# Optimization experiments

Hardware: AMD Instinct MI355X
Metric: run time of the kernel (lower is better)

The kernel has to match this reference:

```python
import jax, jax.numpy as jnp
import numpy as np

N = 50000
NEG_SLOPE = 0.2


def gat_conv(x, src, dst, W, a_src, a_dst, b):
    # PyG GATConv, heads=1: h = xW; e_ij = LeakyReLU(a_src.h_j + a_dst.h_i);
    # softmax over edges sharing destination i; out_i = sum_j alpha_ij h_j + b.
    h = x @ W                                   # [N, F]
    as_ = h @ a_src                             # [N]
    ad_ = h @ a_dst                             # [N]
    e = jax.nn.leaky_relu(as_[src] + ad_[dst], NEG_SLOPE)  # [E]
    m = jax.ops.segment_max(e, dst, num_segments=N)        # per-dst max
    m = jnp.where(jnp.isfinite(m), m, 0.0)
    p = jnp.exp(e - m[dst])
    denom = jax.ops.segment_sum(p, dst, num_segments=N)
    alpha = p / jnp.maximum(denom[dst], 1e-16)             # [E]
    out = jax.ops.segment_sum(alpha[:, None] * h[src], dst, num_segments=N)
    return out + b


def setup_inputs() -> dict:
    key = jax.random.key(0)
    ks = jax.random.split(key, 12)
    E, L = 800000, 262144
    F_in, F_mid, F_out = 128, 64, 32
    x = jax.random.normal(ks[0], (N, F_in), dtype=jnp.float32)
    edge_index = jax.random.randint(ks[1], (2, E), 0, N, dtype=jnp.int32)
    edge_label_index = jax.random.randint(ks[2], (2, L), 0, N, dtype=jnp.int32)
    s1 = 1.0 / np.sqrt(F_in)
    s2 = 1.0 / np.sqrt(F_mid)
    return {
        "x": x,
        "edge_index": edge_index,
        "edge_label_index": edge_label_index,
        "W1": jax.random.normal(ks[3], (F_in, F_mid), jnp.float32) * s1,
        "a_src1": jax.random.normal(ks[4], (F_mid,), jnp.float32) * s2,
        "a_dst1": jax.random.normal(ks[5], (F_mid,), jnp.float32) * s2,
        "b1": jnp.zeros((F_mid,), jnp.float32),
        "W2": jax.random.normal(ks[6], (F_mid, F_out), jnp.float32) * s2,
        "a_src2": jax.random.normal(ks[7], (F_out,), jnp.float32) * (1.0 / np.sqrt(F_out)),
        "a_dst2": jax.random.normal(ks[8], (F_out,), jnp.float32) * (1.0 / np.sqrt(F_out)),
        "b2": jnp.zeros((F_out,), jnp.float32),
    }


def reference(x, edge_index, edge_label_index, W1, a_src1, a_dst1, b1, W2, a_src2, a_dst2, b2):
    # add self-loops (PyG GATConv default add_self_loops=True)
    loops = jnp.arange(N, dtype=edge_index.dtype)
    src = jnp.concatenate([edge_index[0], loops])
    dst = jnp.concatenate([edge_index[1], loops])
    z = jax.nn.relu(gat_conv(x, src, dst, W1, a_src1, a_dst1, b1))
    z = gat_conv(z, src, dst, W2, a_src2, a_dst2, b2)
    # dot-product decode over candidate edges
    return jnp.sum(z[edge_label_index[0]] * z[edge_label_index[1]], axis=-1)
```

## Files before the change

### kernel.cpp

```cpp
#include <hip/hip_runtime.h>

#define NN 50000
#define NEG 0.2f
#define NBUCK 196
#define NBLK 208
#define SLOT 64

__device__ __forceinline__ float leaky(float v) { return v > 0.0f ? v : NEG * v; }

__device__ __forceinline__ unsigned f2bf(float x) {
    unsigned u = __float_as_uint(x);
    return (u + 0x7FFFu + ((u >> 16) & 1u)) >> 16;
}
__device__ __forceinline__ float bflo(unsigned g) { return __uint_as_float(g << 16); }
__device__ __forceinline__ float bfhi(unsigned g) { return __uint_as_float(g & 0xFFFF0000u); }

__global__ __launch_bounds__(256) void k_part_gemm1(
        const int* __restrict__ ei, int E, int CHUNK,
        int* __restrict__ bh, unsigned int* __restrict__ part,
        const float* __restrict__ x, const float* __restrict__ W,
        const float* __restrict__ a_src, const float* __restrict__ a_dst,
        unsigned int* __restrict__ hu, float* __restrict__ as_, float* __restrict__ ad_) {
    __shared__ float xs[4][8][128];
    __shared__ int hist[NBUCK];
    int tid = threadIdx.x;
    if (blockIdx.x < NBLK) {
        int b = blockIdx.x;
        if (tid < NBUCK) hist[tid] = 0;
        __syncthreads();
        int beg = b * CHUNK;
        int end = min(beg + CHUNK, E);
        for (int i = beg + tid; i < end; i += 256) {
            int sv = ei[i], dv = ei[E + i];
            int k = dv >> 8;
            int slot = atomicAdd(&hist[k], 1);
            if (slot < SLOT)
                part[(k * NBLK + b) * SLOT + slot] =
                    (unsigned)sv | ((unsigned)(dv & 255) << 16);
        }
        __syncthreads();
        if (tid < NBUCK) bh[b * NBUCK + tid] = min(hist[tid], SLOT);
        return;
    }
    int gblock = blockIdx.x - NBLK;
    int wl = tid >> 6;
    int lane = tid & 63;
    int base = (gblock * 4 + wl) * 8;
    if (base >= NN) return;
#pragma unroll
    for (int n = 0; n < 8; ++n) {
        int node = base + n;
        xs[wl][n][lane]      = x[node * 128 + lane];
        xs[wl][n][lane + 64] = x[node * 128 + 64 + lane];
    }
    float acc[8] = {0, 0, 0, 0, 0, 0, 0, 0};
#pragma unroll 8
    for (int kg = 0; kg < 32; ++kg) {
        float w0 = W[(4 * kg + 0) * 64 + lane];
        float w1 = W[(4 * kg + 1) * 64 + lane];
        float w2 = W[(4 * kg + 2) * 64 + lane];
        float w3 = W[(4 * kg + 3) * 64 + lane];
#pragma unroll
        for (int n = 0; n < 8; ++n) {
            float4 xv = *(const float4*)&xs[wl][n][kg * 4];
            acc[n] = fmaf(xv.x, w0, fmaf(xv.y, w1, fmaf(xv.z, w2, fmaf(xv.w, w3, acc[n]))));
        }
    }
    float pa = a_src[lane], pd = a_dst[lane];
#pragma unroll
    for (int n = 0; n < 8; ++n) {
        int node = base + n;
        unsigned my = f2bf(acc[n]);
        unsigned nb = __shfl_down(my, 1, 64);
        if ((lane & 1) == 0) hu[node * 32 + (lane >> 1)] = my | (nb << 16);
        float s = acc[n] * pa;
        float d = acc[n] * pd;
#pragma unroll
        for (int off = 32; off > 0; off >>= 1) {
            s += __shfl_xor(s, off, 64);
            d += __shfl_xor(d, off, 64);
        }
        if (lane == 0) { as_[node] = s; ad_[node] = d; }
    }
}

__global__ __launch_bounds__(256) void k_csr(
        const unsigned int* __restrict__ part, const int* __restrict__ bh,
        int2* __restrict__ rc, unsigned short* __restrict__ csr_src) {
    int k = blockIdx.x;
    int tid = threadIdx.x;
    int dst = (k << 8) + tid;
    __shared__ int lhist[256], roff[256], wsum[4];
    lhist[tid] = (dst < NN) ? 1 : 0;
    __syncthreads();
    int rl = 0;
    const unsigned int* myslot = part;
    if (tid < NBLK) {
        rl = bh[tid * NBUCK + k];
        myslot = part + (k * NBLK + tid) * SLOT;
        for (int i = 0; i < rl; ++i) atomicAdd(&lhist[myslot[i] >> 16], 1);
    }
    __syncthreads();
    int lane = tid & 63, w = tid >> 6;
    int v = lhist[tid];
    int inc = v;
#pragma unroll
    for (int off = 1; off < 64; off <<= 1) {
        int t = __shfl_up(inc, off, 64);
        if (lane >= off) inc += t;
    }
    if (lane == 63) wsum[w] = inc;
    __syncthreads();
    int wpre = 0;
    for (int q = 0; q < w; ++q) wpre += wsum[q];
    int excl = wpre + inc - v;
    int cbase = k * NBLK * SLOT;
    roff[tid] = cbase + excl;
    if (dst < NN) rc[dst] = make_int2(cbase + excl, v);
    __syncthreads();
    if (dst < NN) {
        int pos = atomicAdd(&roff[tid], 1);
        csr_src[pos] = (unsigned short)dst;
    }
    if (tid < NBLK) {
        for (int i = 0; i < rl; ++i) {
            unsigned e = myslot[i];
            int pos = atomicAdd(&roff[e >> 16], 1);
            csr_src[pos] = (unsigned short)(e & 0xFFFFu);
        }
    }
}

__global__ __launch_bounds__(256) void k_aggr1g2(
        const int2* __restrict__ rc, const unsigned short* __restrict__ csr_src,
        const float* __restrict__ as_, const float* __restrict__ ad_,
        const unsigned int* __restrict__ hu, const float* __restrict__ b1,
        const float* __restrict__ W2, const float* __restrict__ a2s,
        const float* __restrict__ a2d,
        unsigned int* __restrict__ hu2, float* __restrict__ as2,
        float* __restrict__ ad2) {
    __shared__ float w2s[64 * 32];
    int tid = threadIdx.x;
#pragma unroll
    for (int i = 0; i < 8; ++i) w2s[tid + 256 * i] = W2[tid + 256 * i];
    __syncthreads();
    int f = tid & 15;
    int dst = blockIdx.x * 16 + (tid >> 4);
    int2 rcv = rc[dst];
    int start = rcv.x, deg = rcv.y;
    float ad = ad_[dst];
    float a0 = 0, a1 = 0, a2 = 0, a3 = 0, ssum;

    if (deg <= 32) {
        int nA = min(deg, 16);
        int sA = 0, sB = 0;
        float eA = -1e30f, eB = -1e30f;
        if (f < nA) { sA = csr_src[start + f]; eA = leaky(as_[sA] + ad); }
        if (16 + f < deg) { sB = csr_src[start + 16 + f]; eB = leaky(as_[sB] + ad); }
        float m = fmaxf(eA, eB);
#pragma unroll
        for (int off = 8; off > 0; off >>= 1) m = fmaxf(m, __shfl_xor(m, off, 16));
        float pA = (f < nA) ? __expf(eA - m) : 0.0f;
        float pB = (16 + f < deg) ? __expf(eB - m) : 0.0f;
        ssum = pA + pB;
#pragma unroll
        for (int off = 8; off > 0; off >>= 1) ssum += __shfl_xor(ssum, off, 16);
        int t = 0;
        for (; t + 4 <= nA; t += 4) {
            int s0 = __shfl(sA, t, 16), s1 = __shfl(sA, t + 1, 16);
            int s2 = __shfl(sA, t + 2, 16), s3 = __shfl(sA, t + 3, 16);
            float p0 = __shfl(pA, t, 16), p1 = __shfl(pA, t + 1, 16);
            float p2 = __shfl(pA, t + 2, 16), p3 = __shfl(pA, t + 3, 16);
            uint2 g0 = *(const uint2*)&hu[s0 * 32 + 2 * f];
            uint2 g1 = *(const uint2*)&hu[s1 * 32 + 2 * f];
            uint2 g2 = *(const uint2*)&hu[s2 * 32 + 2 * f];
            uint2 g3 = *(const uint2*)&hu[s3 * 32 + 2 * f];
            a0 = fmaf(p0, bflo(g0.x), a0); a1 = fmaf(p0, bfhi(g0.x), a1);
            a2 = fmaf(p0, bflo(g0.y), a2); a3 = fmaf(p0, bfhi(g0.y), a3);
            a0 = fmaf(p1, bflo(g1.x), a0); a1 = fmaf(p1, bfhi(g1.x), a1);
            a2 = fmaf(p1, bflo(g1.y), a2); a3 = fmaf(p1, bfhi(g1.y), a3);
            a0 = fmaf(p2, bflo(g2.x), a0); a1 = fmaf(p2, bfhi(g2.x), a1);
            a2 = fmaf(p2, bflo(g2.y), a2); a3 = fmaf(p2, bfhi(g2.y), a3);
            a0 = fmaf(p3, bflo(g3.x), a0); a1 = fmaf(p3, bfhi(g3.x), a1);
            a2 = fmaf(p3, bflo(g3.y), a2); a3 = fmaf(p3, bfhi(g3.y), a3);
        }
        for (; t < nA; ++t) {
            int sv = __shfl(sA, t, 16);
            float pv = __shfl(pA, t, 16);
            uint2 g = *(const uint2*)&hu[sv * 32 + 2 * f];
            a0 = fmaf(pv, bflo(g.x), a0); a1 = fmaf(pv, bfhi(g.x), a1);
            a2 = fmaf(pv, bflo(g.y), a2); a3 = fmaf(pv, bfhi(g.y), a3);
        }
        for (t = 16; t < deg; ++t) {
            int sv = __shfl(sB, t - 16, 16);
            float pv = __shfl(pB, t - 16, 16);
            uint2 g = *(const uint2*)&hu[sv * 32 + 2 * f];
            a0 = fmaf(pv, bflo(g.x), a0); a1 = fmaf(pv, bfhi(g.x), a1);
            a2 = fmaf(pv, bflo(g.y), a2); a3 = fmaf(pv, bfhi(g.y), a3);
        }
    } else {
        float m = -1e30f;
        for (int base = 0; base < deg; base += 16) {
            int j = base + f;
            if (j < deg) m = fmaxf(m, leaky(as_[csr_src[start + j]] + ad));
        }
#pragma unroll
        for (int off = 8; off > 0; off >>= 1) m = fmaxf(m, __shfl_xor(m, off, 16));
        ssum = 0.0f;
        for (int base = 0; base < deg; base += 16) {
            int j = base + f;
            int sj = 0;
            float pj = 0.0f;
            if (j < deg) {
                sj = csr_src[start + j];
                pj = __expf(leaky(as_[sj] + ad) - m);
            }
            ssum += pj;
            int lim = min(16, deg - base);
            for (int t = 0; t < lim; ++t) {
                int sv = __shfl(sj, t, 16);
                float pv = __shfl(pj, t, 16);
                uint2 g = *(const uint2*)&hu[sv * 32 + 2 * f];
                a0 = fmaf(pv, bflo(g.x), a0); a1 = fmaf(pv, bfhi(g.x), a1);
                a2 = fmaf(pv, bflo(g.y), a2); a3 = fmaf(pv, bfhi(g.y), a3);
            }
        }
#pragma unroll
        for (int off = 8; off > 0; off >>= 1) ssum += __shfl_xor(ssum, off, 16);
    }

    float inv = 1.0f / ssum;
    float4 bb = *(const float4*)&b1[4 * f];
    float z0 = fmaxf(fmaf(a0, inv, bb.x), 0.0f);
    float z1 = fmaxf(fmaf(a1, inv, bb.y), 0.0f);
    float z2 = fmaxf(fmaf(a2, inv, bb.z), 0.0f);
    float z3 = fmaxf(fmaf(a3, inv, bb.w), 0.0f);

    float h0 = 0.0f, h1 = 0.0f;
#pragma unroll 4
    for (int t = 0; t < 16; ++t) {
        float y0 = __shfl(z0, t, 16);
        float y1 = __shfl(z1, t, 16);
        float y2 = __shfl(z2, t, 16);
        float y3 = __shfl(z3, t, 16);
        const float2* wp = (const float2*)&w2s[(4 * t) * 32 + 2 * f];
        float2 w0v = wp[0];
        float2 w1v = wp[16];
        float2 w2v = wp[32];
        float2 w3v = wp[48];
        h0 = fmaf(y0, w0v.x, fmaf(y1, w1v.x, fmaf(y2, w2v.x, fmaf(y3, w3v.x, h0))));
        h1 = fmaf(y0, w0v.y, fmaf(y1, w1v.y, fmaf(y2, w2v.y, fmaf(y3, w3v.y, h1))));
    }
    float2 av = *(const float2*)&a2s[2 * f];
    float2 dv = *(const float2*)&a2d[2 * f];
    float sa = fmaf(h0, av.x, h1 * av.y);
    float sd = fmaf(h0, dv.x, h1 * dv.y);
#pragma unroll
    for (int off = 8; off > 0; off >>= 1) {
        sa += __shfl_xor(sa, off, 16);
        sd += __shfl_xor(sd, off, 16);
    }
    if (f == 0) { as2[dst] = sa; ad2[dst] = sd; }
    hu2[dst * 16 + f] = f2bf(h0) | (f2bf(h1) << 16);
}

__global__ void k_aggr2(const int2* __restrict__ rc,
                        const unsigned short* __restrict__ csr_src,
                        const float* __restrict__ as_, const float* __restrict__ ad_,
                        const unsigned int* __restrict__ hu2, const float* __restrict__ b,
                        float* __restrict__ out) {
    int gid = blockIdx.x * blockDim.x + threadIdx.x;
    int dst = gid >> 4;
    int f = gid & 15;
    if (dst >= NN) return;
    int2 rcv = rc[dst];
    int start = rcv.x, deg = rcv.y;
    float ad = ad_[dst];
    float a0 = 0, a1 = 0, ssum;

    if (deg <= 32) {
        int nA = min(deg, 16);
        int sA = 0, sB = 0;
        float eA = -1e30f, eB = -1e30f;
        if (f < nA) { sA = csr_src[start + f]; eA = leaky(as_[sA] + ad); }
        if (16 + f < deg) { sB = csr_src[start + 16 + f]; eB = leaky(as_[sB] + ad); }
        float m = fmaxf(eA, eB);
#pragma unroll
        for (int off = 8; off > 0; off >>= 1) m = fmaxf(m, __shfl_xor(m, off, 16));
        float pA = (f < nA) ? __expf(eA - m) : 0.0f;
        float pB = (16 + f < deg) ? __expf(eB - m) : 0.0f;
        ssum = pA + pB;
#pragma unroll
        for (int off = 8; off > 0; off >>= 1) ssum += __shfl_xor(ssum, off, 16);
        int t = 0;
        for (; t + 4 <= nA; t += 4) {
            int s0 = __shfl(sA, t, 16), s1 = __shfl(sA, t + 1, 16);
            int s2 = __shfl(sA, t + 2, 16), s3 = __shfl(sA, t + 3, 16);
            float p0 = __shfl(pA, t, 16), p1 = __shfl(pA, t + 1, 16);
            float p2 = __shfl(pA, t + 2, 16), p3 = __shfl(pA, t + 3, 16);
            unsigned g0 = hu2[s0 * 16 + f];
            unsigned g1 = hu2[s1 * 16 + f];
            unsigned g2 = hu2[s2 * 16 + f];
            unsigned g3 = hu2[s3 * 16 + f];
            a0 = fmaf(p0, bflo(g0), a0); a1 = fmaf(p0, bfhi(g0), a1);
            a0 = fmaf(p1, bflo(g1), a0); a1 = fmaf(p1, bfhi(g1), a1);
            a0 = fmaf(p2, bflo(g2), a0); a1 = fmaf(p2, bfhi(g2), a1);
            a0 = fmaf(p3, bflo(g3), a0); a1 = fmaf(p3, bfhi(g3), a1);
        }
        for (; t < nA; ++t) {
            int sv = __shfl(sA, t, 16);
            float pv = __shfl(pA, t, 16);
            unsigned g = hu2[sv * 16 + f];
            a0 = fmaf(pv, bflo(g), a0); a1 = fmaf(pv, bfhi(g), a1);
        }
        for (t = 16; t < deg; ++t) {
            int sv = __shfl(sB, t - 16, 16);
            float pv = __shfl(pB, t - 16, 16);
            unsigned g = hu2[sv * 16 + f];
            a0 = fmaf(pv, bflo(g), a0); a1 = fmaf(pv, bfhi(g), a1);
        }
    } else {
        float m = -1e30f;
        for (int base = 0; base < deg; base += 16) {
            int j = base + f;
            if (j < deg) m = fmaxf(m, leaky(as_[csr_src[start + j]] + ad));
        }
#pragma unroll
        for (int off = 8; off > 0; off >>= 1) m = fmaxf(m, __shfl_xor(m, off, 16));
        ssum = 0.0f;
        for (int base = 0; base < deg; base += 16) {
            int j = base + f;
            int sj = 0;
            float pj = 0.0f;
            if (j < deg) {
                sj = csr_src[start + j];
                pj = __expf(leaky(as_[sj] + ad) - m);
            }
            ssum += pj;
            int lim = min(16, deg - base);
            for (int t = 0; t < lim; ++t) {
                int sv = __shfl(sj, t, 16);
                float pv = __shfl(pj, t, 16);
                unsigned g = hu2[sv * 16 + f];
                a0 = fmaf(pv, bflo(g), a0); a1 = fmaf(pv, bfhi(g), a1);
            }
        }
#pragma unroll
        for (int off = 8; off > 0; off >>= 1) ssum += __shfl_xor(ssum, off, 16);
    }

    float inv = 1.0f / ssum;
    float2 bb = *(const float2*)&b[2 * f];
    float2 r;
    r.x = fmaf(a0, inv, bb.x);
    r.y = fmaf(a1, inv, bb.y);
    *(float2*)&out[dst * 32 + 2 * f] = r;
}

__global__ void k_decode(const int* __restrict__ eli, int L,
                         const float* __restrict__ z2, float* __restrict__ out) {
    int gid = blockIdx.x * blockDim.x + threadIdx.x;
    int pair = gid >> 3;
    int f4 = gid & 7;
    if (pair >= L) return;
    int i = eli[pair];
    int j = eli[L + pair];
    float4 a = *(const float4*)&z2[i * 32 + f4 * 4];
    float4 b = *(const float4*)&z2[j * 32 + f4 * 4];
    float v = a.x * b.x + a.y * b.y + a.z * b.z + a.w * b.w;
#pragma unroll
    for (int off = 4; off > 0; off >>= 1) v += __shfl_xor(v, off, 8);
    if (f4 == 0) out[pair] = v;
}

extern "C" void kernel_launch(void* const* d_in, const int* in_sizes, int n_in,
                              void* d_out, int out_size, void* d_ws, size_t ws_size,
                              hipStream_t stream) {
    const float* x     = (const float*)d_in[0];
    const int*   ei    = (const int*)d_in[1];
    const int*   eli   = (const int*)d_in[2];
    const float* W1    = (const float*)d_in[3];
    const float* asrc1 = (const float*)d_in[4];
    const float* adst1 = (const float*)d_in[5];
    const float* b1    = (const float*)d_in[6];
    const float* W2    = (const float*)d_in[7];
    const float* asrc2 = (const float*)d_in[8];
    const float* adst2 = (const float*)d_in[9];
    const float* b2    = (const float*)d_in[10];
    float* out = (float*)d_out;

    const int E = in_sizes[1] / 2;
    const int L = in_sizes[2] / 2;
    const int CHUNK = (E + NBLK - 1) / NBLK;

    float* ws  = (float*)d_ws;
    unsigned int* hu  = (unsigned int*)ws;
    unsigned int* hu2 = hu + NN * 32;
    float* z2  = (float*)(hu2 + NN * 16);
    float* as1 = z2 + NN * 32;
    float* ad1 = as1 + NN;
    float* as2 = ad1 + NN;
    float* ad2 = as2 + NN;
    int2* rc  = (int2*)(ad2 + NN);
    int* bh   = (int*)(rc + NN);
    unsigned int*   part    = (unsigned int*)(bh + NBLK * NBUCK);
    unsigned short* csr_src = (unsigned short*)(part + NBUCK * NBLK * SLOT);

    const int GB = (NN / 8 + 3) / 4;

    k_part_gemm1<<<NBLK + GB, 256, 0, stream>>>(ei, E, CHUNK, bh, part,
                                                x, W1, asrc1, adst1, hu, as1, ad1);
    k_csr<<<NBUCK, 256, 0, stream>>>(part, bh, rc, csr_src);

    k_aggr1g2<<<NN / 16, 256, 0, stream>>>(rc, csr_src, as1, ad1, hu, b1,
                                           W2, asrc2, adst2, hu2, as2, ad2);

    k_aggr2<<<(NN * 16 + 255) / 256, 256, 0, stream>>>(
        rc, csr_src, as2, ad2, hu2, b2, z2);

    k_decode<<<(L * 8 + 255) / 256, 256, 0, stream>>>(eli, L, z2, out);
}
```

Baseline: 196.6 us.

## Merge all five stages into one cooperative persistent kernel with grid syncs

Replaces the five separate launches (partition+GEMM1, CSR build, layer-1 aggregation+GEMM2, layer-2 aggregation, decode) with a single cooperative kernel. Blocks loop over virtual block indices and the stages are separated by grid.sync(). The aim is to remove per-launch overhead and the inter-kernel gaps. In exchange, the grid is capped by occupancy (at most 1536 blocks), shared memory becomes a union sized to the largest stage, and every stage is serialized behind a grid-wide barrier.

```diff
diff --git a/kernel.cpp b/kernel.cpp
--- a/kernel.cpp
+++ b/kernel.cpp
@@ -1,10 +1,14 @@
 #include <hip/hip_runtime.h>
+#include <hip/hip_cooperative_groups.h>
+
+namespace cg = cooperative_groups;
 
 #define NN 50000
 #define NEG 0.2f
 #define NBUCK 196
 #define NBLK 208
 #define SLOT 64
+#define GB1 1563
 
 __device__ __forceinline__ float leaky(float v) { return v > 0.0f ? v : NEG * v; }
 
@@ -15,362 +19,364 @@
 __device__ __forceinline__ float bflo(unsigned g) { return __uint_as_float(g << 16); }
 __device__ __forceinline__ float bfhi(unsigned g) { return __uint_as_float(g & 0xFFFF0000u); }
 
-__global__ __launch_bounds__(256) void k_part_gemm1(
+__global__ __launch_bounds__(256, 6) void k_mega(
         const int* __restrict__ ei, int E, int CHUNK,
-        int* __restrict__ bh, unsigned int* __restrict__ part,
-        const float* __restrict__ x, const float* __restrict__ W,
-        const float* __restrict__ a_src, const float* __restrict__ a_dst,
-        unsigned int* __restrict__ hu, float* __restrict__ as_, float* __restrict__ ad_) {
-    __shared__ float xs[4][8][128];
-    __shared__ int hist[NBUCK];
+        int* __restrict__ bh, unsigned int* __restrict__ part_,
+        const float* __restrict__ x, const float* __restrict__ W1,
+        const float* __restrict__ a1s, const float* __restrict__ a1d,
+        unsigned int* __restrict__ hu, float* __restrict__ as1, float* __restrict__ ad1,
+        int2* __restrict__ rc, unsigned short* __restrict__ csr_src,
+        const float* __restrict__ b1, const float* __restrict__ W2,
+        const float* __restrict__ a2s, const float* __restrict__ a2d,
+        unsigned int* __restrict__ hu2, float* __restrict__ as2, float* __restrict__ ad2,
+        const float* __restrict__ b2, float* __restrict__ z2,
+        const int* __restrict__ eli, int L, float* __restrict__ out) {
+    cg::grid_group grid = cg::this_grid();
+    __shared__ union {
+        float xs[4][8][128];
+        int hist[NBUCK];
+        struct { int lhist[256]; int roff[256]; int wsum[4]; } c;
+        float w2s[64 * 32];
+    } su;
     int tid = threadIdx.x;
-    if (blockIdx.x < NBLK) {
-        int b = blockIdx.x;
-        if (tid < NBUCK) hist[tid] = 0;
+
+    for (int vb = blockIdx.x; vb < NBLK + GB1; vb += gridDim.x) {
         __syncthreads();
-        int beg = b * CHUNK;
-        int end = min(beg + CHUNK, E);
-        for (int i = beg + tid; i < end; i += 256) {
-            int sv = ei[i], dv = ei[E + i];
-            int k = dv >> 8;
-            int slot = atomicAdd(&hist[k], 1);
-            if (slot < SLOT)
-                part[(k * NBLK + b) * SLOT + slot] =
-                    (unsigned)sv | ((unsigned)(dv & 255) << 16);
-        }
+        if (vb < NBLK) {
+            if (tid < NBUCK) su.hist[tid] = 0;
+            __syncthreads();
+            int beg = vb * CHUNK, end = min(beg + CHUNK, E);
+            for (int i = beg + tid; i < end; i += 256) {
+                int sv = ei[i], dv = ei[E + i];
+                int k = dv >> 8;
+                int slot = atomicAdd(&su.hist[k], 1);
+                if (slot < SLOT)
+                    part_[(k * NBLK + vb) * SLOT + slot] =
+                        (unsigned)sv | ((unsigned)(dv & 255) << 16);
+            }
+            __syncthreads();
+            if (tid < NBUCK) bh[vb * NBUCK + tid] = min(su.hist[tid], SLOT);
+        } else {
+            int gb = vb - NBLK;
+            int wl = tid >> 6, lane = tid & 63;
+            int base = (gb * 4 + wl) * 8;
+            if (base < NN) {
+#pragma unroll
+                for (int n = 0; n < 8; ++n) {
+                    int node = base + n;
+                    su.xs[wl][n][lane]      = x[node * 128 + lane];
+                    su.xs[wl][n][lane + 64] = x[node * 128 + 64 + lane];
+                }
+                float acc[8] = {0, 0, 0, 0, 0, 0, 0, 0};
+#pragma unroll 8
+                for (int kg = 0; kg < 32; ++kg) {
+                    float w0 = W1[(4 * kg + 0) * 64 + lane];
+                    float w1 = W1[(4 * kg + 1) * 64 + lane];
+                    float w2 = W1[(4 * kg + 2) * 64 + lane];
+                    float w3 = W1[(4 * kg + 3) * 64 + lane];
+#pragma unroll
+                    for (int n = 0; n < 8; ++n) {
+                        float4 xv = *(const float4*)&su.xs[wl][n][kg * 4];
+                        acc[n] = fmaf(xv.x, w0, fmaf(xv.y, w1, fmaf(xv.z, w2, fmaf(xv.w, w3, acc[n]))));
+                    }
+                }
+                float pa = a1s[lane], pd = a1d[lane];
+#pragma unroll
+                for (int n = 0; n < 8; ++n) {
+                    int node = base + n;
+                    unsigned my = f2bf(acc[n]);
+                    unsigned nb = __shfl_down(my, 1, 64);
+                    if ((lane & 1) == 0) hu[node * 32 + (lane >> 1)] = my | (nb << 16);
+                    float s = acc[n] * pa;
+                    float d = acc[n] * pd;
+#pragma unroll
+                    for (int off = 32; off > 0; off >>= 1) {
+                        s += __shfl_xor(s, off, 64);
+                        d += __shfl_xor(d, off, 64);
+                    }
+                    if (lane == 0) { as1[node] = s; ad1[node] = d; }
+                }
+            }
+        }
+    }
+    grid.sync();
+
+    if (blockIdx.x < NBUCK) {
+        int k = blockIdx.x;
+        int dst = (k << 8) + tid;
+        su.c.lhist[tid] = (dst < NN) ? 1 : 0;
         __syncthreads();
-        if (tid < NBUCK) bh[b * NBUCK + tid] = min(hist[tid], SLOT);
-        return;
+        int rl = 0;
+        const unsigned int* myslot = part_;
+        if (tid < NBLK) {
+            rl = bh[tid * NBUCK + k];
+            myslot = part_ + (k * NBLK + tid) * SLOT;
+            for (int i = 0; i < rl; ++i) atomicAdd(&su.c.lhist[myslot[i] >> 16], 1);
+        }
+        __syncthreads();
+        int lane = tid & 63, w = tid >> 6;
+        int v = su.c.lhist[tid];
+        int inc = v;
+#pragma unroll
+        for (int off = 1; off < 64; off <<= 1) {
+            int t = __shfl_up(inc, off, 64);
+            if (lane >= off) inc += t;
+        }
+        if (lane == 63) su.c.wsum[w] = inc;
+        __syncthreads();
+        int wpre = 0;
+        for (int q = 0; q < w; ++q) wpre += su.c.wsum[q];
+        int excl = wpre + inc - v;
+        int cbase = k * NBLK * SLOT;
+        su.c.roff[tid] = cbase + excl;
+        if (dst < NN) rc[dst] = make_int2(cbase + excl, v);
+        __syncthreads();
+        if (dst < NN) {
+            int pos = atomicAdd(&su.c.roff[tid], 1);
+            csr_src[pos] = (unsigned short)dst;
+        }
+        if (tid < NBLK) {
+            for (int i = 0; i < rl; ++i) {
+                unsigned e = myslot[i];
+                int pos = atomicAdd(&su.c.roff[e >> 16], 1);
+                csr_src[pos] = (unsigned short)(e & 0xFFFFu);
+            }
+        }
     }
-    int gblock = blockIdx.x - NBLK;
-    int wl = tid >> 6;
-    int lane = tid & 63;
-    int base = (gblock * 4 + wl) * 8;
-    if (base >= NN) return;
-#pragma unroll
-    for (int n = 0; n < 8; ++n) {
-        int node = base + n;
-        xs[wl][n][lane]      = x[node * 128 + lane];
-        xs[wl][n][lane + 64] = x[node * 128 + 64 + lane];
+    grid.sync();
+
+#pragma unroll
+    for (int i = 0; i < 8; ++i) su.w2s[tid + 256 * i] = W2[tid + 256 * i];
+    __syncthreads();
+    {
+        int f = tid & 15;
+        for (int vb = blockIdx.x; vb < NN / 16; vb += gridDim.x) {
+            int dst = vb * 16 + (tid >> 4);
+            int2 rcv = rc[dst];
+            int start = rcv.x, deg = rcv.y;
+            float ad = ad1[dst];
+            float a0 = 0, a1 = 0, a2 = 0, a3 = 0, ssum;
+
+            if (deg <= 32) {
+                int nA = min(deg, 16);
+                int sA = 0, sB = 0;
+                float eA = -1e30f, eB = -1e30f;
+                if (f < nA) { sA = csr_src[start + f]; eA = leaky(as1[sA] + ad); }
+                if (16 + f < deg) { sB = csr_src[start + 16 + f]; eB = leaky(as1[sB] + ad); }
+                float m = fmaxf(eA, eB);
+#pragma unroll
+                for (int off = 8; off > 0; off >>= 1) m = fmaxf(m, __shfl_xor(m, off, 16));
+                float pA = (f < nA) ? __expf(eA - m) : 0.0f;
+                float pB = (16 + f < deg) ? __expf(eB - m) : 0.0f;
+                ssum = pA + pB;
+#pragma unroll
+                for (int off = 8; off > 0; off >>= 1) ssum += __shfl_xor(ssum, off, 16);
+                int t = 0;
+                for (; t + 4 <= nA; t += 4) {
+                    int s0 = __shfl(sA, t, 16), s1 = __shfl(sA, t + 1, 16);
+                    int s2 = __shfl(sA, t + 2, 16), s3 = __shfl(sA, t + 3, 16);
+                    float p0 = __shfl(pA, t, 16), p1 = __shfl(pA, t + 1, 16);
+                    float p2 = __shfl(pA, t + 2, 16), p3 = __shfl(pA, t + 3, 16);
+                    uint2 g0 = *(const uint2*)&hu[s0 * 32 + 2 * f];
+                    uint2 g1 = *(const uint2*)&hu[s1 * 32 + 2 * f];
+                    uint2 g2 = *(const uint2*)&hu[s2 * 32 + 2 * f];
+                    uint2 g3 = *(const uint2*)&hu[s3 * 32 + 2 * f];
+                    a0 = fmaf(p0, bflo(g0.x), a0); a1 = fmaf(p0, bfhi(g0.x), a1);
+                    a2 = fmaf(p0, bflo(g0.y), a2); a3 = fmaf(p0, bfhi(g0.y), a3);
+                    a0 = fmaf(p1, bflo(g1.x), a0); a1 = fmaf(p1, bfhi(g1.x), a1);
+                    a2 = fmaf(p1, bflo(g1.y), a2); a3 = fmaf(p1, bfhi(g1.y), a3);
+                    a0 = fmaf(p2, bflo(g2.x), a0); a1 = fmaf(p2, bfhi(g2.x), a1);
+                    a2 = fmaf(p2, bflo(g2.y), a2); a3 = fmaf(p2, bfhi(g2.y), a3);
+                    a0 = fmaf(p3, bflo(g3.x), a0); a1 = fmaf(p3, bfhi(g3.x), a1);
+                    a2 = fmaf(p3, bflo(g3.y), a2); a3 = fmaf(p3, bfhi(g3.y), a3);
+                }
+                for (; t < nA; ++t) {
+                    int sv = __shfl(sA, t, 16);
+                    float pv = __shfl(pA, t, 16);
+                    uint2 g = *(const uint2*)&hu[sv * 32 + 2 * f];
+                    a0 = fmaf(pv, bflo(g.x), a0); a1 = fmaf(pv, bfhi(g.x), a1);
+                    a2 = fmaf(pv, bflo(g.y), a2); a3 = fmaf(pv, bfhi(g.y), a3);
+                }
+                for (t = 16; t < deg; ++t) {
+                    int sv = __shfl(sB, t - 16, 16);
+                    float pv = __shfl(pB, t - 16, 16);
+                    uint2 g = *(const uint2*)&hu[sv * 32 + 2 * f];
+                    a0 = fmaf(pv, bflo(g.x), a0); a1 = fmaf(pv, bfhi(g.x), a1);
+                    a2 = fmaf(pv, bflo(g.y), a2); a3 = fmaf(pv, bfhi(g.y), a3);
+                }
+            } else {
+                float m = -1e30f;
+                for (int base = 0; base < deg; base += 16) {
+                    int j = base + f;
+                    if (j < deg) m = fmaxf(m, leaky(as1[csr_src[start + j]] + ad));
+                }
+#pragma unroll
+                for (int off = 8; off > 0; off >>= 1) m = fmaxf(m, __shfl_xor(m, off, 16));
+                ssum = 0.0f;
+                for (int base = 0; base < deg; base += 16) {
+                    int j = base + f;
+                    int sj = 0;
+                    float pj = 0.0f;
+                    if (j < deg) {
+                        sj = csr_src[start + j];
+                        pj = __expf(leaky(as1[sj] + ad) - m);
+                    }
+                    ssum += pj;
+                    int lim = min(16, deg - base);
+                    for (int t = 0; t < lim; ++t) {
+                        int sv = __shfl(sj, t, 16);
+                        float pv = __shfl(pj, t, 16);
+                        uint2 g = *(const uint2*)&hu[sv * 32 + 2 * f];
+                        a0 = fmaf(pv, bflo(g.x), a0); a1 = fmaf(pv, bfhi(g.x), a1);
+                        a2 = fmaf(pv, bflo(g.y), a2); a3 = fmaf(pv, bfhi(g.y), a3);
+                    }
+                }
+#pragma unroll
+                for (int off = 8; off > 0; off >>= 1) ssum += __shfl_xor(ssum, off, 16);
+            }
+
+            float inv = 1.0f / ssum;
+            float4 bb = *(const float4*)&b1[4 * f];
+            float z0 = fmaxf(fmaf(a0, inv, bb.x), 0.0f);
+            float z1 = fmaxf(fmaf(a1, inv, bb.y), 0.0f);
+            float zz2 = fmaxf(fmaf(a2, inv, bb.z), 0.0f);
+            float z3 = fmaxf(fmaf(a3, inv, bb.w), 0.0f);
+
+            float h0 = 0.0f, h1 = 0.0f;
+#pragma unroll 4
+            for (int t = 0; t < 16; ++t) {
+                float y0 = __shfl(z0, t, 16);
+                float y1 = __shfl(z1, t, 16);
+                float y2 = __shfl(zz2, t, 16);
+                float y3 = __shfl(z3, t, 16);
+                const float2* wp = (const float2*)&su.w2s[(4 * t) * 32 + 2 * f];
+                float2 w0v = wp[0];
+                float2 w1v = wp[16];
+                float2 w2v = wp[32];
+                float2 w3v = wp[48];
+                h0 = fmaf(y0, w0v.x, fmaf(y1, w1v.x, fmaf(y2, w2v.x, fmaf(y3, w3v.x, h0))));
+                h1 = fmaf(y0, w0v.y, fmaf(y1, w1v.y, fmaf(y2, w2v.y, fmaf(y3, w3v.y, h1))));
+            }
+            float2 av = *(const float2*)&a2s[2 * f];
+            float2 dv = *(const float2*)&a2d[2 * f];
+            float sa = fmaf(h0, av.x, h1 * av.y);
+            float sd = fmaf(h0, dv.x, h1 * dv.y);
+#pragma unroll
+            for (int off = 8; off > 0; off >>= 1) {
+                sa += __shfl_xor(sa, off, 16);
+                sd += __shfl_xor(sd, off, 16);
+            }
+            if (f == 0) { as2[dst] = sa; ad2[dst] = sd; }
+            hu2[dst * 16 + f] = f2bf(h0) | (f2bf(h1) << 16);
+        }
     }
-    float acc[8] = {0, 0, 0, 0, 0, 0, 0, 0};
-#pragma unroll 8
-    for (int kg = 0; kg < 32; ++kg) {
-        float w0 = W[(4 * kg + 0) * 64 + lane];
-        float w1 = W[(4 * kg + 1) * 64 + lane];
-        float w2 = W[(4 * kg + 2) * 64 + lane];
-        float w3 = W[(4 * kg + 3) * 64 + lane];
-#pragma unroll
-        for (int n = 0; n < 8; ++n) {
-            float4 xv = *(const float4*)&xs[wl][n][kg * 4];
-            acc[n] = fmaf(xv.x, w0, fmaf(xv.y, w1, fmaf(xv.z, w2, fmaf(xv.w, w3, acc[n]))));
-        }
-    }
-    float pa = a_src[lane], pd = a_dst[lane];
-#pragma unroll
-    for (int n = 0; n < 8; ++n) {
-        int node = base + n;
-        unsigned my = f2bf(acc[n]);
-        unsigned nb = __shfl_down(my, 1, 64);
-        if ((lane & 1) == 0) hu[node * 32 + (lane >> 1)] = my | (nb << 16);
-        float s = acc[n] * pa;
-        float d = acc[n] * pd;
-#pragma unroll
-        for (int off = 32; off > 0; off >>= 1) {
-            s += __shfl_xor(s, off, 64);
-            d += __shfl_xor(d, off, 64);
-        }
-        if (lane == 0) { as_[node] = s; ad_[node] = d; }
-    }
-}
-
-__global__ __launch_bounds__(256) void k_csr(
-        const unsigned int* __restrict__ part, const int* __restrict__ bh,
-        int2* __restrict__ rc, unsigned short* __restrict__ csr_src) {
-    int k = blockIdx.x;
-    int tid = threadIdx.x;
-    int dst = (k << 8) + tid;
-    __shared__ int lhist[256], roff[256], wsum[4];
-    lhist[tid] = (dst < NN) ? 1 : 0;
-    __syncthreads();
-    int rl = 0;
-    const unsigned int* myslot = part;
-    if (tid < NBLK) {
-        rl = bh[tid * NBUCK + k];
-        myslot = part + (k * NBLK + tid) * SLOT;
-        for (int i = 0; i < rl; ++i) atomicAdd(&lhist[myslot[i] >> 16], 1);
-    }
-    __syncthreads();
-    int lane = tid & 63, w = tid >> 6;
-    int v = lhist[tid];
-    int inc = v;
-#pragma unroll
-    for (int off = 1; off < 64; off <<= 1) {
-        int t = __shfl_up(inc, off, 64);
-        if (lane >= off) inc += t;
-    }
-    if (lane == 63) wsum[w] = inc;
-    __syncthreads();
-    int wpre = 0;
-    for (int q = 0; q < w; ++q) wpre += wsum[q];
-    int excl = wpre + inc - v;
-    int cbase = k * NBLK * SLOT;
-    roff[tid] = cbase + excl;
-    if (dst < NN) rc[dst] = make_int2(cbase + excl, v);
-    __syncthreads();
-    if (dst < NN) {
-        int pos = atomicAdd(&roff[tid], 1);
-        csr_src[pos] = (unsigned short)dst;
-    }
-    if (tid < NBLK) {
-        for (int i = 0; i < rl; ++i) {
-            unsigned e = myslot[i];
-            int pos = atomicAdd(&roff[e >> 16], 1);
-            csr_src[pos] = (unsigned short)(e & 0xFFFFu);
-        }
-    }
-}
-
-__global__ __launch_bounds__(256) void k_aggr1g2(
-        const int2* __restrict__ rc, const unsigned short* __restrict__ csr_src,
-        const float* __restrict__ as_, const float* __restrict__ ad_,
-        const unsigned int* __restrict__ hu, const float* __restrict__ b1,
-        const float* __restrict__ W2, const float* __restrict__ a2s,
-        const float* __restrict__ a2d,
-        unsigned int* __restrict__ hu2, float* __restrict__ as2,
-        float* __restrict__ ad2) {
-    __shared__ float w2s[64 * 32];
-    int tid = threadIdx.x;
-#pragma unroll
-    for (int i = 0; i < 8; ++i) w2s[tid + 256 * i] = W2[tid + 256 * i];
-    __syncthreads();
-    int f = tid & 15;
-    int dst = blockIdx.x * 16 + (tid >> 4);
-    int2 rcv = rc[dst];
-    int start = rcv.x, deg = rcv.y;
-    float ad = ad_[dst];
-    float a0 = 0, a1 = 0, a2 = 0, a3 = 0, ssum;
-
-    if (deg <= 32) {
-        int nA = min(deg, 16);
-        int sA = 0, sB = 0;
-        float eA = -1e30f, eB = -1e30f;
-        if (f < nA) { sA = csr_src[start + f]; eA = leaky(as_[sA] + ad); }
-        if (16 + f < deg) { sB = csr_src[start + 16 + f]; eB = leaky(as_[sB] + ad); }
-        float m = fmaxf(eA, eB);
-#pragma unroll
-        for (int off = 8; off > 0; off >>= 1) m = fmaxf(m, __shfl_xor(m, off, 16));
-        float pA = (f < nA) ? __expf(eA - m) : 0.0f;
-        float pB = (16 + f < deg) ? __expf(eB - m) : 0.0f;
-        ssum = pA + pB;
-#pragma unroll
-        for (int off = 8; off > 0; off >>= 1) ssum += __shfl_xor(ssum, off, 16);
-        int t = 0;
-        for (; t + 4 <= nA; t += 4) {
-            int s0 = __shfl(sA, t, 16), s1 = __shfl(sA, t + 1, 16);
-            int s2 = __shfl(sA, t + 2, 16), s3 = __shfl(sA, t + 3, 16);
-            float p0 = __shfl(pA, t, 16), p1 = __shfl(pA, t + 1, 16);
-            float p2 = __shfl(pA, t + 2, 16), p3 = __shfl(pA, t + 3, 16);
-            uint2 g0 = *(const uint2*)&hu[s0 * 32 + 2 * f];
-            uint2 g1 = *(const uint2*)&hu[s1 * 32 + 2 * f];
-            uint2 g2 = *(const uint2*)&hu[s2 * 32 + 2 * f];
-            uint2 g3 = *(const uint2*)&hu[s3 * 32 + 2 * f];
-            a0 = fmaf(p0, bflo(g0.x), a0); a1 = fmaf(p0, bfhi(g0.x), a1);
-            a2 = fmaf(p0, bflo(g0.y), a2); a3 = fmaf(p0, bfhi(g0.y), a3);
-            a0 = fmaf(p1, bflo(g1.x), a0); a1 = fmaf(p1, bfhi(g1.x), a1);
-            a2 = fmaf(p1, bflo(g1.y), a2); a3 = fmaf(p1, bfhi(g1.y), a3);
-            a0 = fmaf(p2, bflo(g2.x), a0); a1 = fmaf(p2, bfhi(g2.x), a1);
-            a2 = fmaf(p2, bflo(g2.y), a2); a3 = fmaf(p2, bfhi(g2.y), a3);
-            a0 = fmaf(p3, bflo(g3.x), a0); a1 = fmaf(p3, bfhi(g3.x), a1);
-            a2 = fmaf(p3, bflo(g3.y), a2); a3 = fmaf(p3, bfhi(g3.y), a3);
-        }
-        for (; t < nA; ++t) {
-            int sv = __shfl(sA, t, 16);
-            float pv = __shfl(pA, t, 16);
-            uint2 g = *(const uint2*)&hu[sv * 32 + 2 * f];
-            a0 = fmaf(pv, bflo(g.x), a0); a1 = fmaf(pv, bfhi(g.x), a1);
-            a2 = fmaf(pv, bflo(g.y), a2); a3 = fmaf(pv, bfhi(g.y), a3);
-        }
-        for (t = 16; t < deg; ++t) {
-            int sv = __shfl(sB, t - 16, 16);
-            float pv = __shfl(pB, t - 16, 16);
-            uint2 g = *(const uint2*)&hu[sv * 32 + 2 * f];
-            a0 = fmaf(pv, bflo(g.x), a0); a1 = fmaf(pv, bfhi(g.x), a1);
-            a2 = fmaf(pv, bflo(g.y), a2); a3 = fmaf(pv, bfhi(g.y), a3);
-        }
-    } else {
-        float m = -1e30f;
-        for (int base = 0; base < deg; base += 16) {
-            int j = base + f;
-            if (j < deg) m = fmaxf(m, leaky(as_[csr_src[start + j]] + ad));
-        }
-#pragma unroll
-        for (int off = 8; off > 0; off >>= 1) m = fmaxf(m, __shfl_xor(m, off, 16));
-        ssum = 0.0f;
-        for (int base = 0; base < deg; base += 16) {
-            int j = base + f;
-            int sj = 0;
-            float pj = 0.0f;
-            if (j < deg) {
-                sj = csr_src[start + j];
-                pj = __expf(leaky(as_[sj] + ad) - m);
-            }
-            ssum += pj;
-            int lim = min(16, deg - base);
-            for (int t = 0; t < lim; ++t) {
-                int sv = __shfl(sj, t, 16);
-                float pv = __shfl(pj, t, 16);
-                uint2 g = *(const uint2*)&hu[sv * 32 + 2 * f];
-                a0 = fmaf(pv, bflo(g.x), a0); a1 = fmaf(pv, bfhi(g.x), a1);
-                a2 = fmaf(pv, bflo(g.y), a2); a3 = fmaf(pv, bfhi(g.y), a3);
-            }
-        }
-#pragma unroll
-        for (int off = 8; off > 0; off >>= 1) ssum += __shfl_xor(ssum, off, 16);
-    }
-
-    float inv = 1.0f / ssum;
-    float4 bb = *(const float4*)&b1[4 * f];
-    float z0 = fmaxf(fmaf(a0, inv, bb.x), 0.0f);
-    float z1 = fmaxf(fmaf(a1, inv, bb.y), 0.0f);
-    float z2 = fmaxf(fmaf(a2, inv, bb.z), 0.0f);
-    float z3 = fmaxf(fmaf(a3, inv, bb.w), 0.0f);
-
-    float h0 = 0.0f, h1 = 0.0f;
-#pragma unroll 4
-    for (int t = 0; t < 16; ++t) {
-        float y0 = __shfl(z0, t, 16);
-        float y1 = __shfl(z1, t, 16);
-        float y2 = __shfl(z2, t, 16);
-        float y3 = __shfl(z3, t, 16);
-        const float2* wp = (const float2*)&w2s[(4 * t) * 32 + 2 * f];
-        float2 w0v = wp[0];
-        float2 w1v = wp[16];
-        float2 w2v = wp[32];
-        float2 w3v = wp[48];
-        h0 = fmaf(y0, w0v.x, fmaf(y1, w1v.x, fmaf(y2, w2v.x, fmaf(y3, w3v.x, h0))));
-        h1 = fmaf(y0, w0v.y, fmaf(y1, w1v.y, fmaf(y2, w2v.y, fmaf(y3, w3v.y, h1))));
-    }
-    float2 av = *(const float2*)&a2s[2 * f];
-    float2 dv = *(const float2*)&a2d[2 * f];
-    float sa = fmaf(h0, av.x, h1 * av.y);
-    float sd = fmaf(h0, dv.x, h1 * dv.y);
-#pragma unroll
-    for (int off = 8; off > 0; off >>= 1) {
-        sa += __shfl_xor(sa, off, 16);
-        sd += __shfl_xor(sd, off, 16);
-    }
-    if (f == 0) { as2[dst] = sa; ad2[dst] = sd; }
-    hu2[dst * 16 + f] = f2bf(h0) | (f2bf(h1) << 16);
-}
-
-__global__ void k_aggr2(const int2* __restrict__ rc,
-                        const unsigned short* __restrict__ csr_src,
-                        const float* __restrict__ as_, const float* __restrict__ ad_,
-                        const unsigned int* __restrict__ hu2, const float* __restrict__ b,
-                        float* __restrict__ out) {
-    int gid = blockIdx.x * blockDim.x + threadIdx.x;
-    int dst = gid >> 4;
-    int f = gid & 15;
-    if (dst >= NN) return;
-    int2 rcv = rc[dst];
-    int start = rcv.x, deg = rcv.y;
-    float ad = ad_[dst];
-    float a0 = 0, a1 = 0, ssum;
-
-    if (deg <= 32) {
-        int nA = min(deg, 16);
-        int sA = 0, sB = 0;
-        float eA = -1e30f, eB = -1e30f;
-        if (f < nA) { sA = csr_src[start + f]; eA = leaky(as_[sA] + ad); }
-        if (16 + f < deg) { sB = csr_src[start + 16 + f]; eB = leaky(as_[sB] + ad); }
-        float m = fmaxf(eA, eB);
-#pragma unroll
-        for (int off = 8; off > 0; off >>= 1) m = fmaxf(m, __shfl_xor(m, off, 16));
-        float pA = (f < nA) ? __expf(eA - m) : 0.0f;
-        float pB = (16 + f < deg) ? __expf(eB - m) : 0.0f;
-        ssum = pA + pB;
-#pragma unroll
-        for (int off = 8; off > 0; off >>= 1) ssum += __shfl_xor(ssum, off, 16);
-        int t = 0;
-        for (; t + 4 <= nA; t += 4) {
-            int s0 = __shfl(sA, t, 16), s1 = __shfl(sA, t + 1, 16);
-            int s2 = __shfl(sA, t + 2, 16), s3 = __shfl(sA, t + 3, 16);
-            float p0 = __shfl(pA, t, 16), p1 = __shfl(pA, t + 1, 16);
-            float p2 = __shfl(pA, t + 2, 16), p3 = __shfl(pA, t + 3, 16);
-            unsigned g0 = hu2[s0 * 16 + f];
-            unsigned g1 = hu2[s1 * 16 + f];
-            unsigned g2 = hu2[s2 * 16 + f];
-            unsigned g3 = hu2[s3 * 16 + f];
-            a0 = fmaf(p0, bflo(g0), a0); a1 = fmaf(p0, bfhi(g0), a1);
-            a0 = fmaf(p1, bflo(g1), a0); a1 = fmaf(p1, bfhi(g1), a1);
-            a0 = fmaf(p2, bflo(g2), a0); a1 = fmaf(p2, bfhi(g2), a1);
-            a0 = fmaf(p3, bflo(g3), a0); a1 = fmaf(p3, bfhi(g3), a1);
-        }
-        for (; t < nA; ++t) {
-            int sv = __shfl(sA, t, 16);
-            float pv = __shfl(pA, t, 16);
-            unsigned g = hu2[sv * 16 + f];
-            a0 = fmaf(pv, bflo(g), a0); a1 = fmaf(pv, bfhi(g), a1);
-        }
-        for (t = 16; t < deg; ++t) {
-            int sv = __shfl(sB, t - 16, 16);
-            float pv = __shfl(pB, t - 16, 16);
-            unsigned g = hu2[sv * 16 + f];
-            a0 = fmaf(pv, bflo(g), a0); a1 = fmaf(pv, bfhi(g), a1);
-        }
-    } else {
-        float m = -1e30f;
-        for (int base = 0; base < deg; base += 16) {
-            int j = base + f;
-            if (j < deg) m = fmaxf(m, leaky(as_[csr_src[start + j]] + ad));
-        }
-#pragma unroll
-        for (int off = 8; off > 0; off >>= 1) m = fmaxf(m, __shfl_xor(m, off, 16));
-        ssum = 0.0f;
-        for (int base = 0; base < deg; base += 16) {
-            int j = base + f;
-            int sj = 0;
-            float pj = 0.0f;
-            if (j < deg) {
-                sj = csr_src[start + j];
-                pj = __expf(leaky(as_[sj] + ad) - m);
-            }
-            ssum += pj;
-            int lim = min(16, deg - base);
-            for (int t = 0; t < lim; ++t) {
-                int sv = __shfl(sj, t, 16);
-                float pv = __shfl(pj, t, 16);
+    grid.sync();
+
+    for (int vb = blockIdx.x; vb < (NN * 16) / 256; vb += gridDim.x) {
+        int gid = vb * 256 + tid;
+        int dst = gid >> 4;
+        int f = gid & 15;
+        int2 rcv = rc[dst];
+        int start = rcv.x, deg = rcv.y;
+        float ad = ad2[dst];
+        float a0 = 0, a1 = 0, ssum;
+
+        if (deg <= 32) {
+            int nA = min(deg, 16);
+            int sA = 0, sB = 0;
+            float eA = -1e30f, eB = -1e30f;
+            if (f < nA) { sA = csr_src[start + f]; eA = leaky(as2[sA] + ad); }
+            if (16 + f < deg) { sB = csr_src[start + 16 + f]; eB = leaky(as2[sB] + ad); }
+            float m = fmaxf(eA, eB);
+#pragma unroll
+            for (int off = 8; off > 0; off >>= 1) m = fmaxf(m, __shfl_xor(m, off, 16));
+            float pA = (f < nA) ? __expf(eA - m) : 0.0f;
+            float pB = (16 + f < deg) ? __expf(eB - m) : 0.0f;
+            ssum = pA + pB;
+#pragma unroll
+            for (int off = 8; off > 0; off >>= 1) ssum += __shfl_xor(ssum, off, 16);
+            int t = 0;
+            for (; t + 4 <= nA; t += 4) {
+                int s0 = __shfl(sA, t, 16), s1 = __shfl(sA, t + 1, 16);
+                int s2 = __shfl(sA, t + 2, 16), s3 = __shfl(sA, t + 3, 16);
+                float p0 = __shfl(pA, t, 16), p1 = __shfl(pA, t + 1, 16);
+                float p2 = __shfl(pA, t + 2, 16), p3 = __shfl(pA, t + 3, 16);
+                unsigned g0 = hu2[s0 * 16 + f];
+                unsigned g1 = hu2[s1 * 16 + f];
+                unsigned g2 = hu2[s2 * 16 + f];
+                unsigned g3 = hu2[s3 * 16 + f];
+                a0 = fmaf(p0, bflo(g0), a0); a1 = fmaf(p0, bfhi(g0), a1);
+                a0 = fmaf(p1, bflo(g1), a0); a1 = fmaf(p1, bfhi(g1), a1);
+                a0 = fmaf(p2, bflo(g2), a0); a1 = fmaf(p2, bfhi(g2), a1);
+                a0 = fmaf(p3, bflo(g3), a0); a1 = fmaf(p3, bfhi(g3), a1);
+            }
+            for (; t < nA; ++t) {
+                int sv = __shfl(sA, t, 16);
+                float pv = __shfl(pA, t, 16);
                 unsigned g = hu2[sv * 16 + f];
                 a0 = fmaf(pv, bflo(g), a0); a1 = fmaf(pv, bfhi(g), a1);
             }
-        }
-#pragma unroll
-        for (int off = 8; off > 0; off >>= 1) ssum += __shfl_xor(ssum, off, 16);
+            for (t = 16; t < deg; ++t) {
+                int sv = __shfl(sB, t - 16, 16);
+                float pv = __shfl(pB, t - 16, 16);
+                unsigned g = hu2[sv * 16 + f];
+                a0 = fmaf(pv, bflo(g), a0); a1 = fmaf(pv, bfhi(g), a1);
+            }
+        } else {
+            float m = -1e30f;
+            for (int base = 0; base < deg; base += 16) {
+                int j = base + f;
+                if (j < deg) m = fmaxf(m, leaky(as2[csr_src[start + j]] + ad));
+            }
+#pragma unroll
+            for (int off = 8; off > 0; off >>= 1) m = fmaxf(m, __shfl_xor(m, off, 16));
+            ssum = 0.0f;
+            for (int base = 0; base < deg; base += 16) {
+                int j = base + f;
+                int sj = 0;
+                float pj = 0.0f;
+                if (j < deg) {
+                    sj = csr_src[start + j];
+                    pj = __expf(leaky(as2[sj] + ad) - m);
+                }
+                ssum += pj;
+                int lim = min(16, deg - base);
+                for (int t = 0; t < lim; ++t) {
+                    int sv = __shfl(sj, t, 16);
+                    float pv = __shfl(pj, t, 16);
+                    unsigned g = hu2[sv * 16 + f];
+                    a0 = fmaf(pv, bflo(g), a0); a1 = fmaf(pv, bfhi(g), a1);
+                }
+            }
+#pragma unroll
+            for (int off = 8; off > 0; off >>= 1) ssum += __shfl_xor(ssum, off, 16);
+        }
+
+        float inv = 1.0f / ssum;
+        float2 bb = *(const float2*)&b2[2 * f];
+        float2 r;
+        r.x = fmaf(a0, inv, bb.x);
+        r.y = fmaf(a1, inv, bb.y);
+        *(float2*)&z2[dst * 32 + 2 * f] = r;
     }
-
-    float inv = 1.0f / ssum;
-    float2 bb = *(const float2*)&b[2 * f];
-    float2 r;
-    r.x = fmaf(a0, inv, bb.x);
-    r.y = fmaf(a1, inv, bb.y);
-    *(float2*)&out[dst * 32 + 2 * f] = r;
-}
-
-__global__ void k_decode(const int* __restrict__ eli, int L,
-                         const float* __restrict__ z2, float* __restrict__ out) {
-    int gid = blockIdx.x * blockDim.x + threadIdx.x;
-    int pair = gid >> 3;
-    int f4 = gid & 7;
-    if (pair >= L) return;
-    int i = eli[pair];
-    int j = eli[L + pair];
-    float4 a = *(const float4*)&z2[i * 32 + f4 * 4];
-    float4 b = *(const float4*)&z2[j * 32 + f4 * 4];
-    float v = a.x * b.x + a.y * b.y + a.z * b.z + a.w * b.w;
-#pragma unroll
-    for (int off = 4; off > 0; off >>= 1) v += __shfl_xor(v, off, 8);
-    if (f4 == 0) out[pair] = v;
+    grid.sync();
+
+    int DV = (L * 8 + 255) >> 8;
+    for (int vb = blockIdx.x; vb < DV; vb += gridDim.x) {
+        int gid = vb * 256 + tid;
+        int pair = gid >> 3;
+        int f4 = gid & 7;
+        if (pair < L) {
+            int i = eli[pair];
+            int j = eli[L + pair];
+            float4 a = *(const float4*)&z2[i * 32 + f4 * 4];
+            float4 b = *(const float4*)&z2[j * 32 + f4 * 4];
+            float v = a.x * b.x + a.y * b.y + a.z * b.z + a.w * b.w;
+#pragma unroll
+            for (int off = 4; off > 0; off >>= 1) v += __shfl_xor(v, off, 8);
+            if (f4 == 0) out[pair] = v;
+        }
+    }
 }
 
 extern "C" void kernel_launch(void* const* d_in, const int* in_sizes, int n_in,
@@ -389,9 +395,9 @@
     const float* b2    = (const float*)d_in[10];
     float* out = (float*)d_out;
 
-    const int E = in_sizes[1] / 2;
-    const int L = in_sizes[2] / 2;
-    const int CHUNK = (E + NBLK - 1) / NBLK;
+    int E = in_sizes[1] / 2;
+    int L = in_sizes[2] / 2;
+    int CHUNK = (E + NBLK - 1) / NBLK;
 
     float* ws  = (float*)d_ws;
     unsigned int* hu  = (unsigned int*)ws;
@@ -406,17 +412,24 @@
     unsigned int*   part    = (unsigned int*)(bh + NBLK * NBUCK);
     unsigned short* csr_src = (unsigned short*)(part + NBUCK * NBLK * SLOT);
 
-    const int GB = (NN / 8 + 3) / 4;
-
-    k_part_gemm1<<<NBLK + GB, 256, 0, stream>>>(ei, E, CHUNK, bh, part,
-                                                x, W1, asrc1, adst1, hu, as1, ad1);
-    k_csr<<<NBUCK, 256, 0, stream>>>(part, bh, rc, csr_src);
-
-    k_aggr1g2<<<NN / 16, 256, 0, stream>>>(rc, csr_src, as1, ad1, hu, b1,
-                                           W2, asrc2, adst2, hu2, as2, ad2);
-
-    k_aggr2<<<(NN * 16 + 255) / 256, 256, 0, stream>>>(
-        rc, csr_src, as2, ad2, hu2, b2, z2);
-
-    k_decode<<<(L * 8 + 255) / 256, 256, 0, stream>>>(eli, L, z2, out);
+    int maxb = 0;
+    if (hipOccupancyMaxActiveBlocksPerMultiprocessor(&maxb, k_mega, 256, 0) != hipSuccess || maxb < 1)
+        maxb = 4;
+    int gridn = maxb * 256;
+    if (gridn > 1536) gridn = 1536;
+    if (gridn < 256)  gridn = 256;
+
+    void* args[] = {
+        (void*)&ei, (void*)&E, (void*)&CHUNK,
+        (void*)&bh, (void*)&part,
+        (void*)&x, (void*)&W1, (void*)&asrc1, (void*)&adst1,
+        (void*)&hu, (void*)&as1, (void*)&ad1,
+        (void*)&rc, (void*)&csr_src,
+        (void*)&b1, (void*)&W2, (void*)&asrc2, (void*)&adst2,
+        (void*)&hu2, (void*)&as2, (void*)&ad2,
+        (void*)&b2, (void*)&z2,
+        (void*)&eli, (void*)&L, (void*)&out,
+    };
+    hipLaunchCooperativeKernel((const void*)k_mega, dim3(gridn), dim3(256),
+                               args, 0, stream);
 }
```

Result: slower. 616.4 us (+213.5%).
